# Kernel optimization log

Hardware: AMD Instinct MI355X
Metric: run time of the kernel (lower is better)

Reference implementation:

```python
import jax, jax.numpy as jnp
import numpy as np

B, N, D, H = 4, 2048, 768, 12
HD = D // H  # head_dim = 64


def setup_inputs() -> dict:
    key = jax.random.key(0)
    k1, k2, k3 = jax.random.split(key, 3)
    z = jax.random.normal(k1, (B, N, D), dtype=jnp.float32)
    # per-head qkv Linear weights, torch Linear convention: y = x @ W.T + b
    Wqkv = jax.random.normal(k2, (H, 3 * HD, D), dtype=jnp.float32) * 0.02
    bqkv = jnp.zeros((H, 3 * HD), dtype=jnp.float32)
    Wmsa = jax.random.normal(k3, (D, D), dtype=jnp.float32) * 0.02
    bmsa = jnp.zeros((D,), dtype=jnp.float32)
    return {"z": z, "Wqkv": Wqkv, "bqkv": bqkv, "Wmsa": Wmsa, "bmsa": bmsa}


def reference(z, Wqkv, bqkv, Wmsa, bmsa):
    # All heads' qkv projections in one einsum: [B,N,D] x [H,3hd,D] -> [B,H,N,3hd]
    qkv = jnp.einsum("bnd,hed->bhne", z, Wqkv) + bqkv[None, :, None, :]
    q, k, v = jnp.split(qkv, 3, axis=-1)  # each [B,H,N,hd]
    scale = 1.0 / jnp.sqrt(jnp.asarray(HD, dtype=z.dtype))
    scores = jnp.einsum("bhqd,bhkd->bhqk", q, k) * scale  # [B,H,N,N]
    attn = jax.nn.softmax(scores, axis=-1)
    out = jnp.einsum("bhqk,bhkd->bhqd", attn, v)  # [B,H,N,hd]
    # concat heads (head order matches the torch per-head cat)
    out = out.transpose(0, 2, 1, 3).reshape(B, N, H * HD)  # [B,N,D]
    return out @ Wmsa.T + bmsa
```

## Files before the change

kernel.cpp:

```cpp
#include <hip/hip_runtime.h>

typedef unsigned short u16;
typedef unsigned int u32;
typedef __attribute__((ext_vector_type(8))) short bf16x8;
typedef __attribute__((ext_vector_type(4))) float f32x4;

#define B_ 4
#define H_ 12
#define N_ 2048
#define D_ 768
#define HD_ 64
#define NTOK (B_ * N_)
#define NE   (H_ * 3 * HD_)

#define BK 64
#define CPITCH 144

#define QSCALE 0.18033688011112042f

__device__ __forceinline__ u16 f2bf(float f) {
    u32 u = __float_as_uint(f);
    u += 0x7fffu + ((u >> 16) & 1u);
    return (u16)(u >> 16);
}

__device__ __forceinline__ f32x4 mfma16(bf16x8 a, bf16x8 b, f32x4 c) {
    return __builtin_amdgcn_mfma_f32_16x16x32_bf16(a, b, c, 0, 0, 0);
}

__device__ __forceinline__ void g2l16(const u16* g, u16* l) {
    __builtin_amdgcn_global_load_lds(
        (const __attribute__((address_space(1))) void*)g,
        (__attribute__((address_space(3))) void*)l, 16, 0, 0);
}

#define NZ4  (NTOK * D_ / 4)
#define NWQ4 (NE * D_ / 4)
#define NWM4 (D_ * D_ / 4)
__global__ __launch_bounds__(256) void cvt_all(const float* __restrict__ z,
                                               const float* __restrict__ Wq,
                                               const float* __restrict__ Wm,
                                               u16* __restrict__ Xbf,
                                               u16* __restrict__ Wqb,
                                               u16* __restrict__ Wmb) {
    int i = blockIdx.x * blockDim.x + threadIdx.x;
    const float* src;
    u16* dst;
    int j;
    if (i < NZ4) {
        src = z; dst = Xbf; j = i;
    } else if (i < NZ4 + NWQ4) {
        src = Wq; dst = Wqb; j = i - NZ4;
    } else if (i < NZ4 + NWQ4 + NWM4) {
        src = Wm; dst = Wmb; j = i - NZ4 - NWQ4;
    } else {
        return;
    }
    float4 v = ((const float4*)src)[j];
    u32 lo = (u32)f2bf(v.x) | ((u32)f2bf(v.y) << 16);
    u32 hi = (u32)f2bf(v.z) | ((u32)f2bf(v.w) << 16);
    ((uint2*)dst)[j] = make_uint2(lo, hi);
}

#define GEMM_CORE(Xp, Wp, TM, SMELEMS)                                         \
    __shared__ u16 smem[SMELEMS];                                              \
    u16* ldsA = smem;                                          \
    u16* ldsB = smem + 2 * (TM) * BK;                         \
    const int tid = threadIdx.x;                                               \
    const int wave = tid >> 6, lane = tid & 63;                                \
    const int lrow = lane & 15, quad = lane >> 4;                              \
    const int flat_ = blockIdx.x;                                              \
    const int mbase = (((flat_ & 7) << 4) | ((flat_ >> 3) & 15)) * (TM);       \
    const int nbase = (flat_ >> 7) * 128;                                      \
    const int srow = tid >> 3;                                      \
    const int schunk = tid & 7;                                                \
    const int sk = (schunk ^ (srow & 7)) << 3;   \
    const int sdst = srow * BK + schunk * 8;     \
    const u16* gA = Xp + (size_t)(mbase + srow) * D_ + sk;                     \
    const u16* gB = Wp + (size_t)(nbase + srow) * D_ + sk;                     \
    const int m_ofs = (wave >> 1) * ((TM) / 2);                                \
    const int n_ofs = (wave & 1) * 64;                                         \
    const int e_ = lrow & 7;                                                   \
    const int offA0 = (m_ofs + lrow) * BK + ((quad ^ e_) << 3);                \
    const int offB0 = (n_ofs + lrow) * BK + ((quad ^ e_) << 3);                \
    f32x4 acc[(TM) / 32][4] = {};                                              \
    _Pragma("unroll") for (int i = 0; i < (TM) / 32; i++)                      \
        g2l16(gA + (size_t)(32 * i) * D_, ldsA + sdst + i * 32 * BK);          \
    _Pragma("unroll") for (int i = 0; i < 4; i++)                              \
        g2l16(gB + (size_t)(32 * i) * D_, ldsB + sdst + i * 32 * BK);          \
    for (int it = 0; it < D_ / BK; it++) {                                     \
        const int cur = it & 1;                                                \
        const int abase = cur * (TM) * BK, bbase = cur * 128 * BK;             \
        __syncthreads();   \
        if (it + 1 < D_ / BK) {                                                \
            const int kt2 = (it + 1) * BK;                                     \
            const int nb = cur ^ 1;                                            \
            _Pragma("unroll") for (int i = 0; i < (TM) / 32; i++)              \
                g2l16(gA + (size_t)(32 * i) * D_ + kt2,                        \
                      ldsA + nb * (TM) * BK + sdst + i * 32 * BK);             \
            _Pragma("unroll") for (int i = 0; i < 4; i++)                      \
                g2l16(gB + (size_t)(32 * i) * D_ + kt2,                        \
                      ldsB + nb * 128 * BK + sdst + i * 32 * BK);              \
        }                                                                      \
        _Pragma("unroll") for (int ks = 0; ks < 2; ks++) {                     \
            const int oa = abase + (offA0 ^ (ks << 5));                       \
            const int ob = bbase + (offB0 ^ (ks << 5));                       \
            bf16x8 af[(TM) / 32], bfr[4];                                      \
            _Pragma("unroll") for (int c = 0; c < (TM) / 32; c++)              \
                af[c] = *(const bf16x8*)&ldsA[oa + c * 16 * BK];               \
            _Pragma("unroll") for (int c = 0; c < 4; c++)                      \
                bfr[c] = *(const bf16x8*)&ldsB[ob + c * 16 * BK];              \
            _Pragma("unroll") for (int i = 0; i < (TM) / 32; i++)              \
                _Pragma("unroll") for (int j = 0; j < 4; j++)                  \
                    acc[i][j] = mfma16(af[i], bfr[j], acc[i][j]);              \
        }                                                                      \
    }

__global__ __launch_bounds__(256) void gemm_qkv(const u16* __restrict__ X,
                                                const u16* __restrict__ W,
                                                const float* __restrict__ bqkv,
                                                u16* __restrict__ Qs,
                                                u16* __restrict__ Ks,
                                                u16* __restrict__ Vt) {
    GEMM_CORE(X, W, 64, 24576)
    __syncthreads();
    u16* ldsC = smem;
#pragma unroll
    for (int cn = 0; cn < 4; cn++) {
        const int E = nbase + n_ofs + cn * 16;
        const int h = E / 192;
        const int rr = E - h * 192;
        const int kind = rr >> 6;
        const float bias = bqkv[E + lrow];
        if (kind == 2) {
            const int d = (rr & 63) + lrow;
#pragma unroll
            for (int cm = 0; cm < 2; cm++) {
                const int t0 = mbase + m_ofs + cm * 16 + quad * 4;
                const int b_ = t0 >> 11, n0 = t0 & (N_ - 1);
                const size_t bh = (size_t)(b_ * H_ + h);
                uint2 pk;
                pk.x = (u32)f2bf(acc[cm][cn][0] + bias) |
                       ((u32)f2bf(acc[cm][cn][1] + bias) << 16);
                pk.y = (u32)f2bf(acc[cm][cn][2] + bias) |
                       ((u32)f2bf(acc[cm][cn][3] + bias) << 16);
                *(uint2*)&Vt[(bh * HD_ + d) * N_ + n0] = pk;
            }
        } else {
            const int fcol = n_ofs + cn * 16 + lrow;
            const float scale = (kind == 0) ? QSCALE : 1.0f;
#pragma unroll
            for (int cm = 0; cm < 2; cm++)
#pragma unroll
                for (int r = 0; r < 4; r++) {
                    const int tok = m_ofs + cm * 16 + quad * 4 + r;
                    ldsC[tok * CPITCH + fcol] =
                        f2bf((acc[cm][cn][r] + bias) * scale);
                }
        }
    }
    __syncthreads();
    {
        const int tok = tid >> 2, sub = tid & 3;
        const int fh = sub >> 1, jh = sub & 1;
        const int gf = nbase + fh * 64;
        const int kind2 = (gf >> 6) % 3;
        if (kind2 != 2) {
            const int h2 = gf / 192;
            const int t = mbase + tok;
            const int b2 = t >> 11, n2 = t & (N_ - 1);
            u16* dst = (kind2 == 0 ? Qs : Ks) +
                       ((size_t)(b2 * H_ + h2) * N_ + n2) * HD_;
            const u16* src = &ldsC[tok * CPITCH + fh * 64];
#pragma unroll
            for (int j = 0; j < 4; j++)
                *(uint4*)&dst[(jh * 4 + j) * 8] =
                    *(const uint4*)&src[(jh * 4 + j) * 8];
        }
    }
}

__global__ __launch_bounds__(256) void gemm_out(const u16* __restrict__ X2,
                                                const u16* __restrict__ W,
                                                const float* __restrict__ bmsa,
                                                float* __restrict__ out) {
    GEMM_CORE(X2, W, 64, 24576)
#pragma unroll
    for (int cn = 0; cn < 4; cn++) {
        const int col = nbase + n_ofs + cn * 16 + lrow;
        const float bias = bmsa[col];
#pragma unroll
        for (int cm = 0; cm < 2; cm++) {
#pragma unroll
            for (int r = 0; r < 4; r++) {
                const int t = mbase + m_ofs + cm * 16 + quad * 4 + r;
                out[(size_t)t * D_ + col] = acc[cm][cn][r] + bias;
            }
        }
    }
}

__global__ __launch_bounds__(256, 3) void flash_attn(const u16* __restrict__ Qs,
                                                     const u16* __restrict__ Ks,
                                                     const u16* __restrict__ Vt,
                                                     u16* __restrict__ X2) {
    __shared__ u16 ldsK[2][64 * HD_];
    __shared__ u16 ldsV[2][64 * HD_];
    __shared__ u16 ldsP[4][2][16][68];
    const int tid = threadIdx.x;
    const int wave = tid >> 6, lane = tid & 63;
    const int lrow = lane & 15, quad = lane >> 4;
    const int qbase = blockIdx.x * 128 + wave * 32;
    const int bh = blockIdx.y;
    const int b = bh / H_, h = bh - b * H_;

    const u16* Kb = Ks + (size_t)bh * N_ * HD_;
    const u16* Vb = Vt + (size_t)bh * HD_ * N_;

    const int srow = tid >> 3;
    const int schunk = tid & 7;
    const int skk = (schunk ^ (srow & 7)) << 3;
    const int sdst = srow * HD_ + schunk * 8;

    bf16x8 qa[2][2];
#pragma unroll
    for (int t = 0; t < 2; t++) {
        const u16* Qb = Qs + ((size_t)bh * N_ + qbase + t * 16 + lrow) * HD_ + quad * 8;
        qa[t][0] = *(const bf16x8*)(Qb);
        qa[t][1] = *(const bf16x8*)(Qb + 32);
    }

    const int fofs = (quad ^ (lrow & 7)) << 3;
    const short onebf = (short)0x3F80;
    const bf16x8 ones = {onebf, onebf, onebf, onebf, onebf, onebf, onebf, onebf};

    f32x4 Oacc[2][4] = {};
    f32x4 lacc[2] = {};

    {
        const u16* gK = Kb + (size_t)srow * HD_ + skk;
        g2l16(gK, &ldsK[0][sdst]);
        g2l16(gK + (size_t)32 * HD_, &ldsK[0][sdst + 32 * HD_]);
        const u16* gV = Vb + (size_t)srow * N_ + skk;
        g2l16(gV, &ldsV[0][sdst]);
        g2l16(gV + (size_t)32 * N_, &ldsV[0][sdst + 32 * HD_]);
    }

    for (int it = 0; it < N_ / 64; it++) {
        const int cur = it & 1;
        __syncthreads();
        if (it + 1 < N_ / 64) {
            const int kt2 = (it + 1) << 6;
            const u16* gK = Kb + (size_t)(kt2 + srow) * HD_ + skk;
            g2l16(gK, &ldsK[cur ^ 1][sdst]);
            g2l16(gK + (size_t)32 * HD_, &ldsK[cur ^ 1][sdst + 32 * HD_]);
            const u16* gV = Vb + (size_t)srow * N_ + kt2 + skk;
            g2l16(gV, &ldsV[cur ^ 1][sdst]);
            g2l16(gV + (size_t)32 * N_, &ldsV[cur ^ 1][sdst + 32 * HD_]);
        }
        bf16x8 kf[8];
#pragma unroll
        for (int c = 0; c < 4; c++) {
            const int o = (c * 16 + lrow) * HD_ + fofs;
            kf[2 * c]     = *(const bf16x8*)&ldsK[cur][o];
            kf[2 * c + 1] = *(const bf16x8*)&ldsK[cur][o ^ 32];
        }
        f32x4 s[2][4] = {};
        __builtin_amdgcn_s_setprio(1);
#pragma unroll
        for (int t = 0; t < 2; t++)
#pragma unroll
            for (int c = 0; c < 4; c++) {
                s[t][c] = mfma16(kf[2 * c], qa[t][0], s[t][c]);
                s[t][c] = mfma16(kf[2 * c + 1], qa[t][1], s[t][c]);
            }
        __builtin_amdgcn_s_setprio(0);
#pragma unroll
        for (int t = 0; t < 2; t++)
#pragma unroll
            for (int c = 0; c < 4; c++) {
                u32 b0 = __float_as_uint(__builtin_amdgcn_exp2f(s[t][c][0]));
                u32 b1 = __float_as_uint(__builtin_amdgcn_exp2f(s[t][c][1]));
                u32 b2 = __float_as_uint(__builtin_amdgcn_exp2f(s[t][c][2]));
                u32 b3 = __float_as_uint(__builtin_amdgcn_exp2f(s[t][c][3]));
                uint2 pk;
                pk.x = __builtin_amdgcn_perm(b1, b0, 0x07060302u);
                pk.y = __builtin_amdgcn_perm(b3, b2, 0x07060302u);
                *(uint2*)&ldsP[wave][t][lrow][c * 16 + quad * 4] = pk;
            }
        bf16x8 pa[2][2];
#pragma unroll
        for (int t = 0; t < 2; t++) {
            pa[t][0] = *(const bf16x8*)&ldsP[wave][t][lrow][quad * 8];
            pa[t][1] = *(const bf16x8*)&ldsP[wave][t][lrow][32 + quad * 8];
        }
        __builtin_amdgcn_s_setprio(1);
#pragma unroll
        for (int t = 0; t < 2; t++) {
            lacc[t] = mfma16(pa[t][0], ones, lacc[t]);
            lacc[t] = mfma16(pa[t][1], ones, lacc[t]);
        }
#pragma unroll
        for (int c = 0; c < 4; c++) {
            const int o = (c * 16 + lrow) * HD_ + fofs;
            bf16x8 v0 = *(const bf16x8*)&ldsV[cur][o];
            bf16x8 v1 = *(const bf16x8*)&ldsV[cur][o ^ 32];
#pragma unroll
            for (int t = 0; t < 2; t++) {
                Oacc[t][c] = mfma16(pa[t][0], v0, Oacc[t][c]);
                Oacc[t][c] = mfma16(pa[t][1], v1, Oacc[t][c]);
            }
        }
        __builtin_amdgcn_s_setprio(0);
    }
#pragma unroll
    for (int t = 0; t < 2; t++)
#pragma unroll
        for (int r = 0; r < 4; r++) {
            const float inv = 1.0f / lacc[t][r];
            const int qrow = qbase + t * 16 + quad * 4 + r;
#pragma unroll
            for (int c = 0; c < 4; c++) {
                X2[((size_t)b * N_ + qrow) * D_ + h * HD_ + c * 16 + lrow] =
                    f2bf(Oacc[t][c][r] * inv);
            }
        }
}

extern "C" void kernel_launch(void* const* d_in, const int* in_sizes, int n_in,
                              void* d_out, int out_size, void* d_ws, size_t ws_size,
                              hipStream_t stream) {
    const float* z    = (const float*)d_in[0];
    const float* Wqkv = (const float*)d_in[1];
    const float* bqkv = (const float*)d_in[2];
    const float* Wmsa = (const float*)d_in[3];
    const float* bmsa = (const float*)d_in[4];
    float* out = (float*)d_out;

    u16* Xbf = (u16*)d_ws;
    u16* Wqb = Xbf + (size_t)NTOK * D_;
    u16* Wmb = Wqb + (size_t)NE * D_;
    u16* Qs  = Wmb + (size_t)D_ * D_;
    u16* Ks  = Qs + (size_t)B_ * H_ * N_ * HD_;
    u16* Vt  = Ks + (size_t)B_ * H_ * N_ * HD_;
    u16* X2  = Vt + (size_t)B_ * H_ * N_ * HD_;

    const int ntot = NZ4 + NWQ4 + NWM4;
    cvt_all<<<(ntot + 255) / 256, 256, 0, stream>>>(z, Wqkv, Wmsa, Xbf, Wqb, Wmb);

    gemm_qkv<<<dim3((NTOK / 64) * (NE / 128)), 256, 0, stream>>>(Xbf, Wqb, bqkv, Qs, Ks, Vt);
    flash_attn<<<dim3(N_ / 128, B_ * H_), 256, 0, stream>>>(Qs, Ks, Vt, X2);
    gemm_out<<<dim3((NTOK / 64) * (D_ / 128)), 256, 0, stream>>>(X2, Wmb, bmsa, out);
}
```

Measured before the change: 203.8 us.

## Restructure GEMM mainloop into 4-stage BK=32 pipeline with single barrier per step

Replaces the double-buffered BK=64 GEMM core with a 4-buffer ring of BK=32 tiles, prefetching three tiles ahead via global_load_lds. Each step uses a partial vmcnt wait and one raw barrier, so several loads stay in flight while the MFMAs run. The LDS swizzle is reworked for 32-wide rows, and both GEMM kernels now declare launch bounds of 3 blocks per CU. In exchange there are twice as many iterations, each with fewer MFMAs, and the clamped tail prefetch re-reads the last tile redundantly.

```diff
diff --git a/kernel.cpp b/kernel.cpp
--- a/kernel.cpp
+++ b/kernel.cpp
@@ -13,7 +13,7 @@
 #define NTOK (B_ * N_)
 #define NE   (H_ * 3 * HD_)
 
-#define BK 64
+#define NT_ 24
 #define CPITCH 144
 
 #define QSCALE 0.18033688011112042f
@@ -62,67 +62,70 @@
     ((uint2*)dst)[j] = make_uint2(lo, hi);
 }
 
-#define GEMM_CORE(Xp, Wp, TM, SMELEMS)                                         \
-    __shared__ u16 smem[SMELEMS];                                              \
-    u16* ldsA = smem;                                          \
-    u16* ldsB = smem + 2 * (TM) * BK;                         \
+#define GEMM_CORE_P(Xp, Wp)                                                    \
+    __shared__ u16 smem[24576];         \
+    u16* ldsA = smem;                                           \
+    u16* ldsB = smem + 4 * 2048;                                \
     const int tid = threadIdx.x;                                               \
     const int wave = tid >> 6, lane = tid & 63;                                \
     const int lrow = lane & 15, quad = lane >> 4;                              \
     const int flat_ = blockIdx.x;                                              \
-    const int mbase = (((flat_ & 7) << 4) | ((flat_ >> 3) & 15)) * (TM);       \
+    const int mbase = (((flat_ & 7) << 4) | ((flat_ >> 3) & 15)) * 64;         \
     const int nbase = (flat_ >> 7) * 128;                                      \
-    const int srow = tid >> 3;                                      \
-    const int schunk = tid & 7;                                                \
-    const int sk = (schunk ^ (srow & 7)) << 3;   \
-    const int sdst = srow * BK + schunk * 8;     \
-    const u16* gA = Xp + (size_t)(mbase + srow) * D_ + sk;                     \
-    const u16* gB = Wp + (size_t)(nbase + srow) * D_ + sk;                     \
-    const int m_ofs = (wave >> 1) * ((TM) / 2);                                \
+    const int rowl = tid >> 2, ch = tid & 3;                                   \
+    const int ksw = (ch ^ ((rowl >> 1) & 3)) << 3;                             \
+    const u16* gAt = Xp + (size_t)(mbase + rowl) * D_ + ksw;                   \
+    const u16* gBt = Wp + (size_t)(nbase + rowl) * D_ + ksw;                   \
+    const int sda = rowl * 32 + ch * 8;        \
+    const int m_ofs = (wave >> 1) * 32;                                        \
     const int n_ofs = (wave & 1) * 64;                                         \
-    const int e_ = lrow & 7;                                                   \
-    const int offA0 = (m_ofs + lrow) * BK + ((quad ^ e_) << 3);                \
-    const int offB0 = (n_ofs + lrow) * BK + ((quad ^ e_) << 3);                \
-    f32x4 acc[(TM) / 32][4] = {};                                              \
-    _Pragma("unroll") for (int i = 0; i < (TM) / 32; i++)                      \
-        g2l16(gA + (size_t)(32 * i) * D_, ldsA + sdst + i * 32 * BK);          \
-    _Pragma("unroll") for (int i = 0; i < 4; i++)                              \
-        g2l16(gB + (size_t)(32 * i) * D_, ldsB + sdst + i * 32 * BK);          \
-    for (int it = 0; it < D_ / BK; it++) {                                     \
-        const int cur = it & 1;                                                \
-        const int abase = cur * (TM) * BK, bbase = cur * 128 * BK;             \
-        __syncthreads();   \
-        if (it + 1 < D_ / BK) {                                                \
-            const int kt2 = (it + 1) * BK;                                     \
-            const int nb = cur ^ 1;                                            \
-            _Pragma("unroll") for (int i = 0; i < (TM) / 32; i++)              \
-                g2l16(gA + (size_t)(32 * i) * D_ + kt2,                        \
-                      ldsA + nb * (TM) * BK + sdst + i * 32 * BK);             \
-            _Pragma("unroll") for (int i = 0; i < 4; i++)                      \
-                g2l16(gB + (size_t)(32 * i) * D_ + kt2,                        \
-                      ldsB + nb * 128 * BK + sdst + i * 32 * BK);              \
+    const int swz = (quad ^ ((lrow >> 1) & 3)) << 3;                           \
+    const int offA = (m_ofs + lrow) * 32 + swz;                                \
+    const int offB = (n_ofs + lrow) * 32 + swz;                                \
+    f32x4 acc[2][4] = {};                                                      \
+    _Pragma("unroll") for (int p = 0; p < 3; p++) {                            \
+        g2l16(gAt + p * 32, ldsA + p * 2048 + sda);                            \
+        g2l16(gBt + p * 32, ldsB + p * 4096 + sda);                            \
+        g2l16(gBt + (size_t)64 * D_ + p * 32, ldsB + p * 4096 + 2048 + sda);   \
+    }                                                                          \
+    _Pragma("unroll 4") for (int t = 0; t < NT_; t++) {                        \
+        asm volatile("s_waitcnt vmcnt(6)" ::: "memory");                       \
+        __builtin_amdgcn_s_barrier();                                          \
+        asm volatile("" ::: "memory");                                         \
+        {                                                                      \
+            const int ts = (t + 3 < NT_) ? (t + 3) : (NT_ - 1);                \
+            const int sb = (t + 3) & 3;                                        \
+            g2l16(gAt + ts * 32, ldsA + sb * 2048 + sda);                      \
+            g2l16(gBt + ts * 32, ldsB + sb * 4096 + sda);                      \
+            g2l16(gBt + (size_t)64 * D_ + ts * 32,                             \
+                  ldsB + sb * 4096 + 2048 + sda);                              \
         }                                                                      \
-        _Pragma("unroll") for (int ks = 0; ks < 2; ks++) {                     \
-            const int oa = abase + (offA0 ^ (ks << 5));                       \
-            const int ob = bbase + (offB0 ^ (ks << 5));                       \
-            bf16x8 af[(TM) / 32], bfr[4];                                      \
-            _Pragma("unroll") for (int c = 0; c < (TM) / 32; c++)              \
-                af[c] = *(const bf16x8*)&ldsA[oa + c * 16 * BK];               \
-            _Pragma("unroll") for (int c = 0; c < 4; c++)                      \
-                bfr[c] = *(const bf16x8*)&ldsB[ob + c * 16 * BK];              \
-            _Pragma("unroll") for (int i = 0; i < (TM) / 32; i++)              \
-                _Pragma("unroll") for (int j = 0; j < 4; j++)                  \
-                    acc[i][j] = mfma16(af[i], bfr[j], acc[i][j]);              \
-        }                                                                      \
-    }
-
-__global__ __launch_bounds__(256) void gemm_qkv(const u16* __restrict__ X,
-                                                const u16* __restrict__ W,
-                                                const float* __restrict__ bqkv,
-                                                u16* __restrict__ Qs,
-                                                u16* __restrict__ Ks,
-                                                u16* __restrict__ Vt) {
-    GEMM_CORE(X, W, 64, 24576)
+        const int ab = (t & 3) * 2048 + offA;                                  \
+        const int bb = (t & 3) * 4096 + offB;                                  \
+        bf16x8 af0 = *(const bf16x8*)&ldsA[ab];                                \
+        bf16x8 af1 = *(const bf16x8*)&ldsA[ab + 16 * 32];                      \
+        bf16x8 bf0 = *(const bf16x8*)&ldsB[bb];                                \
+        bf16x8 bf1 = *(const bf16x8*)&ldsB[bb + 16 * 32];                      \
+        bf16x8 bf2 = *(const bf16x8*)&ldsB[bb + 32 * 32];                      \
+        bf16x8 bf3 = *(const bf16x8*)&ldsB[bb + 48 * 32];                      \
+        acc[0][0] = mfma16(af0, bf0, acc[0][0]);                               \
+        acc[0][1] = mfma16(af0, bf1, acc[0][1]);                               \
+        acc[0][2] = mfma16(af0, bf2, acc[0][2]);                               \
+        acc[0][3] = mfma16(af0, bf3, acc[0][3]);                               \
+        acc[1][0] = mfma16(af1, bf0, acc[1][0]);                               \
+        acc[1][1] = mfma16(af1, bf1, acc[1][1]);                               \
+        acc[1][2] = mfma16(af1, bf2, acc[1][2]);                               \
+        acc[1][3] = mfma16(af1, bf3, acc[1][3]);                               \
+    }                                                                          \
+    asm volatile("s_waitcnt vmcnt(0)" ::: "memory");
+
+__global__ __launch_bounds__(256, 3) void gemm_qkv(const u16* __restrict__ X,
+                                                   const u16* __restrict__ W,
+                                                   const float* __restrict__ bqkv,
+                                                   u16* __restrict__ Qs,
+                                                   u16* __restrict__ Ks,
+                                                   u16* __restrict__ Vt) {
+    GEMM_CORE_P(X, W)
     __syncthreads();
     u16* ldsC = smem;
 #pragma unroll
@@ -180,11 +183,11 @@
     }
 }
 
-__global__ __launch_bounds__(256) void gemm_out(const u16* __restrict__ X2,
-                                                const u16* __restrict__ W,
-                                                const float* __restrict__ bmsa,
-                                                float* __restrict__ out) {
-    GEMM_CORE(X2, W, 64, 24576)
+__global__ __launch_bounds__(256, 3) void gemm_out(const u16* __restrict__ X2,
+                                                   const u16* __restrict__ W,
+                                                   const float* __restrict__ bmsa,
+                                                   float* __restrict__ out) {
+    GEMM_CORE_P(X2, W)
 #pragma unroll
     for (int cn = 0; cn < 4; cn++) {
         const int col = nbase + n_ofs + cn * 16 + lrow;
```

After: 220.8 us. 8.3% more time.
